# Kernel optimization log

Measured on AMD Instinct MI355X. Metric: run time of the kernel, lower is better.

Reference implementation:

```python
import jax, jax.numpy as jnp
import numpy as np

STRIDES = (8, 16, 32)
C = 80          # num_classes
KA = 3          # anchors per level
TOPK = 100      # per-level top-k
CONF_TH = 0.001
NMS_TH = 0.5
INPUT_SIZE = 2048
ANCHOR_SIZES = np.array([[[10, 13], [16, 30], [33, 23]],
                         [[30, 61], [62, 45], [59, 119]],
                         [[116, 90], [156, 198], [373, 326]]], dtype=np.float32)


def make_anchors(level):
    # Mirrors YOLOv3.create_grid: torch.meshgrid default is 'ij' indexing.
    fmp = INPUT_SIZE // STRIDES[level]
    gy, gx = np.meshgrid(np.arange(fmp), np.arange(fmp), indexing='ij')
    grid_xy = np.stack([gx, gy], axis=-1).reshape(-1, 1, 2).astype(np.float32)  # [HW,1,2]
    grid_xy = np.broadcast_to(grid_xy, (fmp * fmp, KA, 2))
    wh = np.broadcast_to(ANCHOR_SIZES[level][None], (fmp * fmp, KA, 2))
    return jnp.asarray(np.concatenate([grid_xy, wh], axis=-1).reshape(-1, 4))  # [HW*KA,4]


def setup_inputs() -> dict:
    key = jax.random.key(0)
    ks = jax.random.split(key, 9)
    d = {}
    for lvl in range(3):
        N = (INPUT_SIZE // STRIDES[lvl]) ** 2 * KA
        d[f"conf_pred_{lvl + 1}"] = jax.random.normal(ks[3 * lvl], (N, 1), jnp.float32)
        d[f"cls_pred_{lvl + 1}"] = jax.random.normal(ks[3 * lvl + 1], (N, C), jnp.float32)
        d[f"reg_pred_{lvl + 1}"] = jax.random.normal(ks[3 * lvl + 2], (N, 4), jnp.float32) * 0.5
        d[f"anchors_{lvl + 1}"] = make_anchors(lvl)
    return d


def _level(conf, cls, reg, anchors, stride):
    # scores = sigmoid(objectness) * softmax(class logits), flattened over (anchor, class)
    prob = jax.nn.sigmoid(conf) * jax.nn.softmax(cls, axis=-1)      # [N,C]
    scores, idx = jax.lax.top_k(prob.reshape(-1), TOPK)             # [TOPK]
    valid = scores > CONF_TH
    a_idx = idx // C
    labels = idx % C
    r = reg[a_idx]                                                  # [TOPK,4]
    a = anchors[a_idx]                                              # [TOPK,4]
    # decode_boxes: xy = (sigmoid(txy)+grid)*stride ; wh = exp(twh)*anchor_wh
    xy = (jax.nn.sigmoid(r[:, :2]) + a[:, :2]) * stride
    wh = jnp.exp(r[:, 2:]) * a[:, 2:]
    boxes = jnp.concatenate([xy - 0.5 * wh, xy + 0.5 * wh], axis=-1)  # x1y1x2y2
    return scores, labels, boxes, valid


def reference(conf_pred_1, cls_pred_1, reg_pred_1,
              conf_pred_2, cls_pred_2, reg_pred_2,
              conf_pred_3, cls_pred_3, reg_pred_3,
              anchors_1, anchors_2, anchors_3):
    levels = [(conf_pred_1, cls_pred_1, reg_pred_1, anchors_1, STRIDES[0]),
              (conf_pred_2, cls_pred_2, reg_pred_2, anchors_2, STRIDES[1]),
              (conf_pred_3, cls_pred_3, reg_pred_3, anchors_3, STRIDES[2])]
    parts = [_level(*lv) for lv in levels]
    scores = jnp.concatenate([p[0] for p in parts])   # [3*TOPK]
    labels = jnp.concatenate([p[1] for p in parts])
    boxes = jnp.concatenate([p[2] for p in parts], axis=0)
    valid = jnp.concatenate([p[3] for p in parts])

    # Sort all candidates by score descending (greedy NMS order)
    order = jnp.argsort(-scores)
    scores, labels, boxes, valid = scores[order], labels[order], boxes[order], valid[order]

    x1, y1, x2, y2 = boxes[:, 0], boxes[:, 1], boxes[:, 2], boxes[:, 3]
    areas = (x2 - x1) * (y2 - y1)
    xx1 = jnp.maximum(x1[:, None], x1[None, :])
    yy1 = jnp.maximum(y1[:, None], y1[None, :])
    xx2 = jnp.minimum(x2[:, None], x2[None, :])
    yy2 = jnp.minimum(y2[:, None], y2[None, :])
    w = jnp.maximum(1e-10, xx2 - xx1)
    h = jnp.maximum(1e-10, yy2 - yy1)
    inter = w * h
    iou = inter / (areas[:, None] + areas[None, :] - inter)

    K = scores.shape[0]
    idxr = jnp.arange(K)
    # class-wise suppression: only same-label, lower-scored boxes can be suppressed
    sup_cond = (iou > NMS_TH) & (labels[:, None] == labels[None, :]) & (idxr[None, :] > idxr[:, None])

    def body(i, keep):
        return keep & ~(sup_cond[i] & keep[i])

    keep = jax.lax.fori_loop(0, K, body, valid)

    boxes_n = jnp.clip(boxes / INPUT_SIZE, 0.0, 1.0)
    out = jnp.concatenate([boxes_n, scores[:, None], labels.astype(jnp.float32)[:, None]], axis=1)
    return jnp.where(keep[:, None], out, 0.0)   # [3*TOPK, 6] = (x1,y1,x2,y2,score,label)
```

## Files before the change

kernel.cpp:

```cpp
#include <hip/hip_runtime.h>
#include <math.h>
#include <stdint.h>

#define NBUCKET 4096
#define NCOPY   8
#define CAP     16384
#define QCAP    4096
#define STAGE   4096
#define FCAP    1024
#define TOPK    100
#define NLVL    3
#define NCLS    80

#define PA_G1 1024
#define PA_G2 256
#define PA_G3 64
#define CK_G1 192
#define CK_G2 48
#define CK_G3 12

__global__ void zero_kernel(uint4* __restrict__ p, unsigned int* __restrict__ ctr)
{
    p[blockIdx.x * 256 + threadIdx.x] = make_uint4(0u, 0u, 0u, 0u);
    if (blockIdx.x == 0 && threadIdx.x == 0) { ctr[0] = 0u; ctr[1] = 0u; }
}

__global__ void passA_kernel(const float* __restrict__ conf1, const float* __restrict__ cls1,
                             const float* __restrict__ conf2, const float* __restrict__ cls2,
                             const float* __restrict__ conf3, const float* __restrict__ cls3,
                             int n1, int n2, int n3,
                             unsigned int* __restrict__ ghist,
                             float* __restrict__ amax)
{
    const float* conf; const float* cls; int nA, nb, b;
    unsigned int* gh; float* am;
    if (blockIdx.x < PA_G1) {
        b = blockIdx.x; conf = conf1; cls = cls1; nA = n1; nb = PA_G1;
        gh = ghist; am = amax;
    } else if (blockIdx.x < PA_G1 + PA_G2) {
        b = blockIdx.x - PA_G1; conf = conf2; cls = cls2; nA = n2; nb = PA_G2;
        gh = ghist + NCOPY * NBUCKET; am = amax + n1;
    } else {
        b = blockIdx.x - PA_G1 - PA_G2; conf = conf3; cls = cls3; nA = n3; nb = PA_G3;
        gh = ghist + 2 * NCOPY * NBUCKET; am = amax + n1 + n2;
    }

    __shared__ unsigned int sh[NBUCKET];
    for (int i = threadIdx.x; i < NBUCKET; i += 256) sh[i] = 0;
    __syncthreads();

    int sub = threadIdx.x & 15;
    int g16 = threadIdx.x >> 4;
    int nChunk = nA >> 4;
    for (int ch = b; ch < nChunk; ch += 2 * nb) {
        int a0 = (ch << 4) + g16;
        int ch1 = ch + nb;
        bool has1 = ch1 < nChunk;
        float cv0 = conf[a0];
        const float* r0 = cls + (size_t)a0 * NCLS + sub;
        float A0 = r0[0], A1 = r0[16], A2 = r0[32], A3 = r0[48], A4 = r0[64];
        float cv1 = 0.0f, B0 = 0, B1 = 0, B2 = 0, B3 = 0, B4 = 0;
        int a1 = 0;
        if (has1) {
            a1 = (ch1 << 4) + g16;
            cv1 = conf[a1];
            const float* r1 = cls + (size_t)a1 * NCLS + sub;
            B0 = r1[0]; B1 = r1[16]; B2 = r1[32]; B3 = r1[48]; B4 = r1[64];
        }
        {
            float sig = 1.0f / (1.0f + expf(-cv0));
            float m = fmaxf(fmaxf(fmaxf(A0, A1), fmaxf(A2, A3)), A4);
#pragma unroll
            for (int o = 8; o >= 1; o >>= 1) m = fmaxf(m, __shfl_xor(m, o, 16));
            float s = ((expf(A0 - m) + expf(A1 - m)) + (expf(A2 - m) + expf(A3 - m))) + expf(A4 - m);
#pragma unroll
            for (int o = 8; o >= 1; o >>= 1) s += __shfl_xor(s, o, 16);
            float inv = sig / s;
            if (sub == 0) {
                am[a0] = inv;
                unsigned bk = __float_as_uint(inv) >> 18;
                if (bk > NBUCKET - 1) bk = NBUCKET - 1;
                atomicAdd(&sh[bk], 1u);
            }
        }
        if (has1) {
            float sig = 1.0f / (1.0f + expf(-cv1));
            float m = fmaxf(fmaxf(fmaxf(B0, B1), fmaxf(B2, B3)), B4);
#pragma unroll
            for (int o = 8; o >= 1; o >>= 1) m = fmaxf(m, __shfl_xor(m, o, 16));
            float s = ((expf(B0 - m) + expf(B1 - m)) + (expf(B2 - m) + expf(B3 - m))) + expf(B4 - m);
#pragma unroll
            for (int o = 8; o >= 1; o >>= 1) s += __shfl_xor(s, o, 16);
            float inv = sig / s;
            if (sub == 0) {
                am[a1] = inv;
                unsigned bk = __float_as_uint(inv) >> 18;
                if (bk > NBUCKET - 1) bk = NBUCKET - 1;
                atomicAdd(&sh[bk], 1u);
            }
        }
    }
    __syncthreads();
    unsigned int* g = gh + (b & (NCOPY - 1)) * NBUCKET;
    for (int i = threadIdx.x; i < NBUCKET; i += 256) {
        unsigned v = sh[i];
        if (v) atomicAdd(&g[i], v);
    }
}

__global__ void scan_kernel(const unsigned int* __restrict__ ghist,
                            unsigned int* __restrict__ thresh,
                            unsigned int* __restrict__ ccount)
{
    int lvl = blockIdx.x;
    const unsigned int* h0 = ghist + lvl * NCOPY * NBUCKET;
    __shared__ unsigned int h[NBUCKET];
    __shared__ unsigned int ps[256];
    int t = threadIdx.x;
    if (t == 0) ccount[lvl] = 0;
    for (int bb = t; bb < NBUCKET; bb += 256) {
        unsigned s = 0;
        for (int c = 0; c < NCOPY; c++) s += h0[c * NBUCKET + bb];
        h[bb] = s;
    }
    __syncthreads();
    unsigned cs = 0;
#pragma unroll
    for (int i = 0; i < 16; i++) cs += h[NBUCKET - 1 - (t * 16 + i)];
    ps[t] = cs;
    __syncthreads();
    for (int o = 1; o < 256; o <<= 1) {
        unsigned v = (t >= o) ? ps[t - o] : 0u;
        __syncthreads();
        ps[t] += v;
        __syncthreads();
    }
    unsigned incl = ps[t], excl = incl - cs;
    if (excl < TOPK && incl >= TOPK) {
        unsigned cum = excl, B = 0;
        for (int i = 0; i < 16; i++) {
            int bb = NBUCKET - 1 - (t * 16 + i);
            cum += h[bb];
            if (cum >= TOPK) { B = (unsigned)bb; break; }
        }
        thresh[lvl] = B << 18;
    }
}

__global__ void compact_kernel(const float* __restrict__ conf1, const float* __restrict__ cls1,
                               const float* __restrict__ conf2, const float* __restrict__ cls2,
                               const float* __restrict__ conf3, const float* __restrict__ cls3,
                               int n1, int n2, int n3,
                               const unsigned int* __restrict__ thresh,
                               const float* __restrict__ amax,
                               unsigned int* __restrict__ ccount,
                               float* __restrict__ cscore,
                               unsigned int* __restrict__ cidx)
{
    const float* conf; const float* cls; int bl, lvl; const float* am;
    if (blockIdx.x < CK_G1)              { lvl = 0; bl = blockIdx.x;               conf = conf1; cls = cls1; am = amax; }
    else if (blockIdx.x < CK_G1 + CK_G2) { lvl = 1; bl = blockIdx.x - CK_G1;       conf = conf2; cls = cls2; am = amax + n1; }
    else                                 { lvl = 2; bl = blockIdx.x - CK_G1 - CK_G2; conf = conf3; cls = cls3; am = amax + n1 + n2; }

    __shared__ int qn;
    __shared__ int queue[QCAP];
    if (threadIdx.x == 0) qn = 0;
    __syncthreads();

    unsigned T = thresh[lvl];
    int idx4 = bl * 256 + threadIdx.x;
    const float4* am4 = (const float4*)am;
    float4 v = am4[idx4];
    float vv[4] = {v.x, v.y, v.z, v.w};
#pragma unroll
    for (int j = 0; j < 4; j++) {
        if (__float_as_uint(vv[j]) >= T) {
            int p = atomicAdd(&qn, 1);
            if (p < QCAP) queue[p] = idx4 * 4 + j;
        }
    }
    __syncthreads();
    int qcnt = min(qn, QCAP);
    int grp = threadIdx.x >> 4;
    int sub = threadIdx.x & 15;
    float*        csl = cscore + lvl * CAP;
    unsigned int* cil = cidx   + lvl * CAP;
    for (int q = grp; q < qcnt; q += 16) {
        int a = queue[q];
        float cv  = conf[a];
        float sig = 1.0f / (1.0f + expf(-cv));
        const float* row = cls + (size_t)a * NCLS + sub;
        float c0 = row[0], c1 = row[16], c2 = row[32], c3 = row[48], c4 = row[64];
        float m = fmaxf(fmaxf(fmaxf(c0, c1), fmaxf(c2, c3)), c4);
#pragma unroll
        for (int o = 8; o >= 1; o >>= 1) m = fmaxf(m, __shfl_xor(m, o, 16));
        float e0 = expf(c0 - m), e1 = expf(c1 - m), e2 = expf(c2 - m),
              e3 = expf(c3 - m), e4 = expf(c4 - m);
        float s = ((e0 + e1) + (e2 + e3)) + e4;
#pragma unroll
        for (int o = 8; o >= 1; o >>= 1) s += __shfl_xor(s, o, 16);
        float inv = sig / s;
        float e[5] = {e0, e1, e2, e3, e4};
#pragma unroll
        for (int k = 0; k < 5; k++) {
            float p = e[k] * inv;
            if (e[k] == 1.0f || __float_as_uint(p) >= T) {
                unsigned pos = atomicAdd(&ccount[lvl], 1u);
                if (pos < CAP) {
                    csl[pos] = p;
                    cil[pos] = (unsigned)(a * NCLS + sub + 16 * k);
                }
            }
        }
    }
}

__device__ __forceinline__ float rlf(float x, int l)
{
    return __uint_as_float((unsigned)__builtin_amdgcn_readlane((int)__float_as_uint(x), l));
}
__device__ __forceinline__ int rli(int x, int l)
{
    return __builtin_amdgcn_readlane(x, l);
}
__device__ __forceinline__ unsigned long long rl64(unsigned long long x, int b)
{
    unsigned lo = (unsigned)__builtin_amdgcn_readlane((int)(unsigned)x, b);
    unsigned hi = (unsigned)__builtin_amdgcn_readlane((int)(unsigned)(x >> 32), b);
    return ((unsigned long long)hi << 32) | lo;
}

__global__ __launch_bounds__(320) void select_prep_kernel(
    const float* __restrict__ cscore, const unsigned int* __restrict__ cidx,
    const unsigned int* __restrict__ ccount,
    const unsigned int* __restrict__ thresh,
    float* __restrict__ sel_sc, int* __restrict__ sel_ix,
    const float* __restrict__ reg1, const float* __restrict__ anch1,
    const float* __restrict__ reg2, const float* __restrict__ anch2,
    const float* __restrict__ reg3, const float* __restrict__ anch3,
    float* __restrict__ t_score, float* __restrict__ t_box,
    int* __restrict__ t_label, int* __restrict__ t_valid,
    unsigned int* __restrict__ sel_done)
{
    int lvl = blockIdx.x;
    int tid = threadIdx.x;
    __shared__ float        q_sc[STAGE];
    __shared__ unsigned int q_ix[STAGE];
    __shared__ unsigned int subh[4096];
    __shared__ unsigned int kthr_s;
    __shared__ int          fcnt;
    __shared__ float        f_sc[FCAP];
    __shared__ unsigned int f_ix[FCAP];
    __shared__ int          lastflag;

    int cnt = min((int)ccount[lvl], CAP);
    const float*        sc = cscore + lvl * CAP;
    const unsigned int* ix = cidx   + lvl * CAP;
    int n = min(cnt, STAGE);
    unsigned B12 = (thresh[lvl] >> 18) << 12;

    for (int i = tid; i < 4096; i += 320) subh[i] = 0;
    if (tid == 0) fcnt = 0;
    for (int c = tid; c < n; c += 320) { q_sc[c] = sc[c]; q_ix[c] = ix[c]; }
    if (tid < TOPK) { sel_sc[lvl * TOPK + tid] = -1e30f; sel_ix[lvl * TOPK + tid] = 0; }
    __syncthreads();

    for (int c = tid; c < cnt; c += 320) {
        float v = (c < n) ? q_sc[c] : sc[c];
        unsigned rel = (__float_as_uint(v) >> 6) - B12;
        if (rel > 4095u) rel = 4095u;
        atomicAdd(&subh[rel], 1u);
    }
    __syncthreads();

    if (tid < 64) {
        int base = 4095 - (tid << 6);
        unsigned csum = 0;
        for (int i = 0; i < 64; i++) csum += subh[base - i];
        unsigned v = csum;
        for (int o = 1; o < 64; o <<= 1) {
            unsigned u = __shfl_up(v, o);
            if (tid >= o) v += u;
        }
        unsigned excl = v - csum;
        if (excl < TOPK && v >= TOPK) {
            unsigned cum = excl;
            for (int i = 0; i < 64; i++) {
                int bb = base - i;
                cum += subh[bb];
                if (cum >= TOPK) { kthr_s = (B12 + (unsigned)bb) << 6; break; }
            }
        }
    }
    __syncthreads();
    unsigned kthr = kthr_s;

    for (int c = tid; c < cnt; c += 320) {
        float v; unsigned vi;
        if (c < n) { v = q_sc[c]; vi = q_ix[c]; }
        else       { v = sc[c];   vi = ix[c];   }
        if (__float_as_uint(v) >= kthr) {
            int p = atomicAdd(&fcnt, 1);
            if (p < FCAP) { f_sc[p] = v; f_ix[p] = vi; }
        }
    }
    __syncthreads();
    int fn = min(fcnt, FCAP);

    for (int c = tid; c < fn; c += 320) {
        float    my  = f_sc[c];
        unsigned myi = f_ix[c];
        int rank = 0;
        for (int k = 0; k < fn; k++) {
            float v = f_sc[k];
            rank += (v > my) || (v == my && f_ix[k] < myi);
        }
        if (rank < TOPK) {
            sel_sc[lvl * TOPK + rank] = my;
            sel_ix[lvl * TOPK + rank] = (int)myi;
        }
    }

    __syncthreads();
    if (tid == 0) {
        __threadfence();
        unsigned prev = atomicAdd(sel_done, 1u);
        lastflag = (prev == NLVL - 1);
    }
    __syncthreads();
    if (!lastflag) return;
    if (tid == 0) __threadfence();
    __syncthreads();

    {
        int lane = tid & 63;
        float sg[5];
#pragma unroll
        for (int g = 0; g < 5; g++) {
            int k = g * 64 + lane;
            sg[g] = (k < 300) ? sel_sc[k] : -INFINITY;
        }
        float my = (tid < 300) ? sel_sc[tid] : -INFINITY;
        int rank = 0;
#pragma unroll
        for (int g = 0; g < 5; g++) {
            int base = g * 64;
#pragma unroll 1
            for (int ii = 0; ii < 64; ii++) {
                float v = rlf(sg[g], ii);
                int k = base + ii;
                rank += (v > my) || (v == my && k < tid);
            }
        }
        if (tid < 300) {
            int lv = tid / TOPK;
            const float* reg = lv == 0 ? reg1 : (lv == 1 ? reg2 : reg3);
            const float* anc = lv == 0 ? anch1 : (lv == 1 ? anch2 : anch3);
            float stride = lv == 0 ? 8.0f : (lv == 1 ? 16.0f : 32.0f);
            int  idx = sel_ix[tid];
            int a   = idx / NCLS;
            int lab = idx % NCLS;
            float r0 = reg[4 * a + 0], r1 = reg[4 * a + 1], r2 = reg[4 * a + 2], r3 = reg[4 * a + 3];
            float a0 = anc[4 * a + 0], a1 = anc[4 * a + 1], a2 = anc[4 * a + 2], a3 = anc[4 * a + 3];
            float cx = (1.0f / (1.0f + expf(-r0)) + a0) * stride;
            float cy = (1.0f / (1.0f + expf(-r1)) + a1) * stride;
            float w  = expf(r2) * a2;
            float h  = expf(r3) * a3;
            t_score[rank]       = my;
            t_box[4 * rank + 0] = cx - 0.5f * w;
            t_box[4 * rank + 1] = cy - 0.5f * h;
            t_box[4 * rank + 2] = cx + 0.5f * w;
            t_box[4 * rank + 3] = cy + 0.5f * h;
            t_label[rank] = lab;
            t_valid[rank] = my > 0.001f;
        }
    }
}

__global__ __launch_bounds__(320) void supnms_kernel(
    const float* __restrict__ t_score, const float* __restrict__ t_box,
    const int* __restrict__ t_label, const int* __restrict__ t_valid,
    unsigned long long* __restrict__ sup_ws,
    unsigned int* __restrict__ sup_done,
    float* __restrict__ out)
{
    int tid  = threadIdx.x;
    int lane = tid & 63;
    int w    = tid >> 6;
    int rbase = 20 * blockIdx.x;
    __shared__ int lastflag;

    float bx1 = 0, by1 = 0, bx2 = 0, by2 = 0, areaj = 0;
    int labj = -1;
    if (tid < 300) {
        bx1 = t_box[4 * tid + 0]; by1 = t_box[4 * tid + 1];
        bx2 = t_box[4 * tid + 2]; by2 = t_box[4 * tid + 3];
        labj = t_label[tid];
        areaj = (bx2 - bx1) * (by2 - by1);
    }

    float rx1 = 0, ry1 = 0, rx2 = 0, ry2 = 0, rar = 1.0f;
    int rlab = -9;
    int r = rbase + lane;
    if (lane < 20 && r < 300) {
        rx1 = t_box[4 * r + 0]; ry1 = t_box[4 * r + 1];
        rx2 = t_box[4 * r + 2]; ry2 = t_box[4 * r + 3];
        rar = (rx2 - rx1) * (ry2 - ry1);
        rlab = t_label[r];
    }

#pragma unroll 1
    for (int ii = 0; ii < 20; ii++) {
        int i = rbase + ii;
        float xi1 = rlf(rx1, ii), yi1 = rlf(ry1, ii);
        float xi2 = rlf(rx2, ii), yi2 = rlf(ry2, ii);
        float ari = rlf(rar, ii);
        int  labi = rli(rlab, ii);
        float xx1 = fmaxf(xi1, bx1), yy1 = fmaxf(yi1, by1);
        float xx2 = fminf(xi2, bx2), yy2 = fminf(yi2, by2);
        float ww = fmaxf(1e-10f, xx2 - xx1);
        float hh = fmaxf(1e-10f, yy2 - yy1);
        float inter = ww * hh;
        float iou = inter / (ari + areaj - inter);
        bool p = (tid > i) && (labj == labi) && (iou > 0.5f) && (tid < 300);
        unsigned long long m = __ballot(p);
        if (lane == 0) sup_ws[i * 5 + w] = m;
    }

    __syncthreads();
    if (tid == 0) {
        __threadfence();
        unsigned prev = atomicAdd(sup_done, 1u);
        lastflag = (prev == 14);
    }
    __syncthreads();
    if (!lastflag) return;
    if (tid == 0) __threadfence();
    __syncthreads();

    if (tid < 64) {
        unsigned long long s0[5], s1[5], s2[5], s3[5], s4[5];
#pragma unroll
        for (int q = 0; q < 5; q++) {
            s0[q] = sup_ws[(lane)       * 5 + q];
            s1[q] = sup_ws[(lane + 64)  * 5 + q];
            s2[q] = sup_ws[(lane + 128) * 5 + q];
            s3[q] = sup_ws[(lane + 192) * 5 + q];
            s4[q] = (lane + 256 < 300) ? sup_ws[(lane + 256) * 5 + q] : 0ull;
        }

        unsigned long long k0 = __ballot(t_valid[lane] != 0);
        unsigned long long k1 = __ballot(t_valid[lane + 64] != 0);
        unsigned long long k2 = __ballot(t_valid[lane + 128] != 0);
        unsigned long long k3 = __ballot(t_valid[lane + 192] != 0);
        unsigned long long k4 = __ballot((lane + 256 < 300) ? (t_valid[lane + 256] != 0) : false);

        unsigned long long nz0 = __ballot((s0[0] | s0[1] | s0[2] | s0[3] | s0[4]) != 0ull);
        unsigned long long nz1 = __ballot((s1[0] | s1[1] | s1[2] | s1[3] | s1[4]) != 0ull);
        unsigned long long nz2 = __ballot((s2[0] | s2[1] | s2[2] | s2[3] | s2[4]) != 0ull);
        unsigned long long nz3 = __ballot((s3[0] | s3[1] | s3[2] | s3[3] | s3[4]) != 0ull);
        unsigned long long nz4 = __ballot((s4[0] | s4[1] | s4[2] | s4[3] | s4[4]) != 0ull);

#define NMS_SPARSE(SR, KR, NZ)                                                \
        {                                                                     \
            unsigned long long m = (NZ);                                      \
            while (m) {                                                       \
                int b = __builtin_ctzll(m);                                   \
                m &= m - 1ull;                                                \
                if ((KR >> b) & 1ull) {                                       \
                    k0 &= ~rl64(SR[0], b);                                    \
                    k1 &= ~rl64(SR[1], b);                                    \
                    k2 &= ~rl64(SR[2], b);                                    \
                    k3 &= ~rl64(SR[3], b);                                    \
                    k4 &= ~rl64(SR[4], b);                                    \
                }                                                             \
            }                                                                 \
        }
        NMS_SPARSE(s0, k0, nz0)
        NMS_SPARSE(s1, k1, nz1)
        NMS_SPARSE(s2, k2, nz2)
        NMS_SPARSE(s3, k3, nz3)
        NMS_SPARSE(s4, k4, nz4)
#undef NMS_SPARSE

#pragma unroll 1
        for (int e = lane; e < 300 * 6; e += 64) {
            int row = e / 6, col = e % 6;
            unsigned long long kw = (row < 64) ? k0 : (row < 128) ? k1 : (row < 192) ? k2
                                  : (row < 256) ? k3 : k4;
            bool kept = (kw >> (row & 63)) & 1ull;
            float v = 0.0f;
            if (kept) {
                if (col < 4) {
                    v = t_box[4 * row + col] * (1.0f / 2048.0f);
                    v = fminf(fmaxf(v, 0.0f), 1.0f);
                } else if (col == 4) {
                    v = t_score[row];
                } else {
                    v = (float)t_label[row];
                }
            }
            out[e] = v;
        }
    }
}

extern "C" void kernel_launch(void* const* d_in, const int* in_sizes, int n_in,
                              void* d_out, int out_size, void* d_ws, size_t ws_size,
                              hipStream_t stream)
{
    const float* conf1 = (const float*)d_in[0];
    const float* cls1  = (const float*)d_in[1];
    const float* reg1  = (const float*)d_in[2];
    const float* anch1 = (const float*)d_in[3];
    const float* conf2 = (const float*)d_in[4];
    const float* cls2  = (const float*)d_in[5];
    const float* reg2  = (const float*)d_in[6];
    const float* anch2 = (const float*)d_in[7];
    const float* conf3 = (const float*)d_in[8];
    const float* cls3  = (const float*)d_in[9];
    const float* reg3  = (const float*)d_in[10];
    const float* anch3 = (const float*)d_in[11];

    int N1 = in_sizes[0];
    int N2 = in_sizes[4];
    int N3 = in_sizes[8];

    unsigned int* wsu    = (unsigned int*)d_ws;
    unsigned int* hist   = wsu;
    unsigned int* thresh = wsu + NLVL * NCOPY * NBUCKET;
    unsigned int* ccount = thresh + NLVL;
    unsigned int* ctrs   = thresh + 6;
    float*        amax   = (float*)(wsu + NLVL * NCOPY * NBUCKET + 16);
    float*        cscore = amax + (N1 + N2 + N3);
    unsigned int* cidx   = (unsigned int*)(cscore + NLVL * CAP);
    float*        sel_sc = (float*)(cidx + NLVL * CAP);
    int*          sel_ix = (int*)(sel_sc + NLVL * TOPK);
    float*        t_score = (float*)(sel_ix + NLVL * TOPK);
    float*        t_box   = t_score + 300;
    int*          t_label = (int*)(t_box + 1200);
    int*          t_valid = t_label + 300;
    unsigned long long* sup_ws =
        (unsigned long long*)(((uintptr_t)(t_valid + 300) + 15) & ~(uintptr_t)15);

    zero_kernel<<<96, 256, 0, stream>>>((uint4*)hist, ctrs);

    passA_kernel<<<PA_G1 + PA_G2 + PA_G3, 256, 0, stream>>>(
        conf1, cls1, conf2, cls2, conf3, cls3, N1, N2, N3, hist, amax);

    scan_kernel<<<NLVL, 256, 0, stream>>>(hist, thresh, ccount);

    compact_kernel<<<CK_G1 + CK_G2 + CK_G3, 256, 0, stream>>>(
        conf1, cls1, conf2, cls2, conf3, cls3, N1, N2, N3,
        thresh, amax, ccount, cscore, cidx);

    select_prep_kernel<<<NLVL, 320, 0, stream>>>(
        cscore, cidx, ccount, thresh, sel_sc, sel_ix,
        reg1, anch1, reg2, anch2, reg3, anch3,
        t_score, t_box, t_label, t_valid, &ctrs[0]);

    supnms_kernel<<<15, 320, 0, stream>>>(
        t_score, t_box, t_label, t_valid, sup_ws, &ctrs[1], (float*)d_out);
}
```

Measured before the change: 95.14 us.

## Stage class logits through LDS with float4 loads; widen select_prep to 1024 threads

In the histogram pass, each wave now loads its four anchor rows of class logits as coalesced float4 vectors into a per-wave LDS buffer. Lanes then read their strided class values from LDS, replacing the earlier per-lane scalar global loads. Separately, select_prep_kernel moves from 320 to 1024 threads, with loop strides updated, and the final merge section is restricted to the first 320 threads. This adds LDS traffic and relies on wave-local ordering without a barrier. The new launch bounds may also limit registers, and the 320-thread guard could clash with any block-wide barriers inside that section.

```diff
diff --git a/kernel.cpp b/kernel.cpp
--- a/kernel.cpp
+++ b/kernel.cpp
@@ -46,33 +46,45 @@
     }
 
     __shared__ unsigned int sh[NBUCKET];
+    __shared__ float4 stg[4][2][80];
     for (int i = threadIdx.x; i < NBUCKET; i += 256) sh[i] = 0;
     __syncthreads();
 
-    int sub = threadIdx.x & 15;
-    int g16 = threadIdx.x >> 4;
+    int wv   = threadIdx.x >> 6;
+    int lane = threadIdx.x & 63;
+    int sub  = threadIdx.x & 15;
+    int g16  = threadIdx.x >> 4;
+    int gloc = g16 & 3;
     int nChunk = nA >> 4;
+
     for (int ch = b; ch < nChunk; ch += 2 * nb) {
-        int a0 = (ch << 4) + g16;
         int ch1 = ch + nb;
         bool has1 = ch1 < nChunk;
+
+        {
+            const float4* src = (const float4*)(cls + (size_t)(ch * 16 + 4 * wv) * NCLS);
+            stg[wv][0][lane] = src[lane];
+            if (lane < 16) stg[wv][0][64 + lane] = src[64 + lane];
+        }
+        if (has1) {
+            const float4* src = (const float4*)(cls + (size_t)(ch1 * 16 + 4 * wv) * NCLS);
+            stg[wv][1][lane] = src[lane];
+            if (lane < 16) stg[wv][1][64 + lane] = src[64 + lane];
+        }
+        int a0 = (ch << 4) + g16;
         float cv0 = conf[a0];
-        const float* r0 = cls + (size_t)a0 * NCLS + sub;
-        float A0 = r0[0], A1 = r0[16], A2 = r0[32], A3 = r0[48], A4 = r0[64];
-        float cv1 = 0.0f, B0 = 0, B1 = 0, B2 = 0, B3 = 0, B4 = 0;
-        int a1 = 0;
-        if (has1) {
-            a1 = (ch1 << 4) + g16;
-            cv1 = conf[a1];
-            const float* r1 = cls + (size_t)a1 * NCLS + sub;
-            B0 = r1[0]; B1 = r1[16]; B2 = r1[32]; B3 = r1[48]; B4 = r1[64];
-        }
+        int a1 = has1 ? (ch1 << 4) + g16 : 0;
+        float cv1 = has1 ? conf[a1] : 0.0f;
+
         {
+            const float* rowl = (const float*)&stg[wv][0][0] + gloc * NCLS;
+            float c0 = rowl[sub], c1 = rowl[sub + 16], c2 = rowl[sub + 32],
+                  c3 = rowl[sub + 48], c4 = rowl[sub + 64];
             float sig = 1.0f / (1.0f + expf(-cv0));
-            float m = fmaxf(fmaxf(fmaxf(A0, A1), fmaxf(A2, A3)), A4);
+            float m = fmaxf(fmaxf(fmaxf(c0, c1), fmaxf(c2, c3)), c4);
 #pragma unroll
             for (int o = 8; o >= 1; o >>= 1) m = fmaxf(m, __shfl_xor(m, o, 16));
-            float s = ((expf(A0 - m) + expf(A1 - m)) + (expf(A2 - m) + expf(A3 - m))) + expf(A4 - m);
+            float s = ((expf(c0 - m) + expf(c1 - m)) + (expf(c2 - m) + expf(c3 - m))) + expf(c4 - m);
 #pragma unroll
             for (int o = 8; o >= 1; o >>= 1) s += __shfl_xor(s, o, 16);
             float inv = sig / s;
@@ -84,11 +96,14 @@
             }
         }
         if (has1) {
+            const float* rowl = (const float*)&stg[wv][1][0] + gloc * NCLS;
+            float c0 = rowl[sub], c1 = rowl[sub + 16], c2 = rowl[sub + 32],
+                  c3 = rowl[sub + 48], c4 = rowl[sub + 64];
             float sig = 1.0f / (1.0f + expf(-cv1));
-            float m = fmaxf(fmaxf(fmaxf(B0, B1), fmaxf(B2, B3)), B4);
+            float m = fmaxf(fmaxf(fmaxf(c0, c1), fmaxf(c2, c3)), c4);
 #pragma unroll
             for (int o = 8; o >= 1; o >>= 1) m = fmaxf(m, __shfl_xor(m, o, 16));
-            float s = ((expf(B0 - m) + expf(B1 - m)) + (expf(B2 - m) + expf(B3 - m))) + expf(B4 - m);
+            float s = ((expf(c0 - m) + expf(c1 - m)) + (expf(c2 - m) + expf(c3 - m))) + expf(c4 - m);
 #pragma unroll
             for (int o = 8; o >= 1; o >>= 1) s += __shfl_xor(s, o, 16);
             float inv = sig / s;
@@ -230,7 +245,7 @@
     return ((unsigned long long)hi << 32) | lo;
 }
 
-__global__ __launch_bounds__(320) void select_prep_kernel(
+__global__ __launch_bounds__(1024, 4) void select_prep_kernel(
     const float* __restrict__ cscore, const unsigned int* __restrict__ cidx,
     const unsigned int* __restrict__ ccount,
     const unsigned int* __restrict__ thresh,
@@ -259,13 +274,13 @@
     int n = min(cnt, STAGE);
     unsigned B12 = (thresh[lvl] >> 18) << 12;
 
-    for (int i = tid; i < 4096; i += 320) subh[i] = 0;
+    for (int i = tid; i < 4096; i += 1024) subh[i] = 0;
     if (tid == 0) fcnt = 0;
-    for (int c = tid; c < n; c += 320) { q_sc[c] = sc[c]; q_ix[c] = ix[c]; }
+    for (int c = tid; c < n; c += 1024) { q_sc[c] = sc[c]; q_ix[c] = ix[c]; }
     if (tid < TOPK) { sel_sc[lvl * TOPK + tid] = -1e30f; sel_ix[lvl * TOPK + tid] = 0; }
     __syncthreads();
 
-    for (int c = tid; c < cnt; c += 320) {
+    for (int c = tid; c < cnt; c += 1024) {
         float v = (c < n) ? q_sc[c] : sc[c];
         unsigned rel = (__float_as_uint(v) >> 6) - B12;
         if (rel > 4095u) rel = 4095u;
@@ -295,7 +310,7 @@
     __syncthreads();
     unsigned kthr = kthr_s;
 
-    for (int c = tid; c < cnt; c += 320) {
+    for (int c = tid; c < cnt; c += 1024) {
         float v; unsigned vi;
         if (c < n) { v = q_sc[c]; vi = q_ix[c]; }
         else       { v = sc[c];   vi = ix[c];   }
@@ -307,7 +322,7 @@
     __syncthreads();
     int fn = min(fcnt, FCAP);
 
-    for (int c = tid; c < fn; c += 320) {
+    for (int c = tid; c < fn; c += 1024) {
         float    my  = f_sc[c];
         unsigned myi = f_ix[c];
         int rank = 0;
@@ -332,7 +347,7 @@
     if (tid == 0) __threadfence();
     __syncthreads();
 
-    {
+    if (tid < 320) {
         int lane = tid & 63;
         float sg[5];
 #pragma unroll
@@ -554,7 +569,7 @@
         conf1, cls1, conf2, cls2, conf3, cls3, N1, N2, N3,
         thresh, amax, ccount, cscore, cidx);
 
-    select_prep_kernel<<<NLVL, 320, 0, stream>>>(
+    select_prep_kernel<<<NLVL, 1024, 0, stream>>>(
         cscore, cidx, ccount, thresh, sel_sc, sel_ix,
         reg1, anch1, reg2, anch2, reg3, anch3,
         t_score, t_box, t_label, t_valid, &ctrs[0]);
```

After: 99.94 us. +5.0%, slower.
